# Kernel tuning notes

Hardware: AMD Instinct MI355X
Metric: run time of the kernel (lower is better)

Reference implementation:

```python
import jax, jax.numpy as jnp
import numpy as np

B = 512        # events (graphs) in batch
NPE = 512      # nodes per event (structured so knn can be batched)
N = B * NPE    # total nodes = 262144
K = 6          # knn neighbors
F_IN = 128     # 2 * n_samples
H = 16         # conv1 out
OUT = 10       # graph_out
COORD_MAX = 16 # detector grid extent


def setup_inputs() -> dict:
    key = jax.random.key(0)
    k1, k2, k3, k4 = jax.random.split(key, 4)
    xy = jax.random.randint(k1, (N, 2), 0, COORD_MAX, dtype=jnp.int32)
    batch = jnp.repeat(jnp.arange(B, dtype=jnp.int32), NPE)  # coo[:,2] = event id
    coo = jnp.concatenate([xy, batch[:, None]], axis=1)       # [N,3] int
    x = jax.random.normal(k2, (N, F_IN), dtype=jnp.float32)
    W1 = jax.random.normal(k3, (F_IN, H), dtype=jnp.float32) * (1.0 / np.sqrt(F_IN))
    b1 = jnp.zeros((H,), dtype=jnp.float32)
    W2 = jax.random.normal(k4, (H, OUT), dtype=jnp.float32) * (1.0 / np.sqrt(H))
    b2 = jnp.zeros((OUT,), dtype=jnp.float32)
    return {"coo": coo, "x": x, "W1": W1, "b1": b1, "W2": W2, "b2": b2}


def knn_edges(coo):
    # knn_graph(coo, K, batch=coo[:,2], loop=False): batches are contiguous
    # blocks of NPE nodes, so reshape and do per-event brute-force knn.
    pos = coo.astype(jnp.float32).reshape(B, NPE, 3)
    # squared pairwise distances per event: [B, n, n]
    d = jnp.sum((pos[:, :, None, :] - pos[:, None, :, :]) ** 2, axis=-1)
    d = d + jnp.eye(NPE, dtype=d.dtype) * 1e9  # exclude self (loop=False)
    _, idx = jax.lax.top_k(-d, K)              # [B, n, K] neighbor indices (local)
    base = (jnp.arange(B, dtype=jnp.int32) * NPE)[:, None, None]
    src = (idx.astype(jnp.int32) + base).reshape(-1)                       # j (neighbor)
    dst = jnp.broadcast_to(jnp.arange(NPE, dtype=jnp.int32)[None, :, None] + base,
                           (B, NPE, K)).reshape(-1)                        # i (center)
    return src, dst


def gcn_conv(x, W, b, src, dst):
    # GCNConv: out = D^{-1/2} (A + I) D^{-1/2} X W + b
    loops = jnp.arange(N, dtype=jnp.int32)
    row = jnp.concatenate([dst, loops])  # target
    col = jnp.concatenate([src, loops])  # source
    deg = jax.ops.segment_sum(jnp.ones_like(row, dtype=x.dtype), row, num_segments=N)
    dinv = jnp.where(deg > 0, jax.lax.rsqrt(deg), 0.0)
    norm = dinv[row] * dinv[col]         # [E]
    h = x @ W                            # [N, F_out]
    msg = h[col] * norm[:, None]         # gather + scale
    return jax.ops.segment_sum(msg, row, num_segments=N) + b


def reference(coo, x, W1, b1, W2, b2):
    src, dst = knn_edges(coo)
    h = jax.nn.relu(gcn_conv(x, W1, b1, src, dst))
    out = gcn_conv(h, W2, b2, src, dst)  # [N, OUT] per-node output (n_lin == 0)
    return out
```

## Files before the change

kernel.cpp:

```cpp
#include <hip/hip_runtime.h>
#include <hip/hip_bf16.h>

#define NPE   512
#define F_IN  128
#define HDIM  16
#define ODIM  10

typedef __attribute__((ext_vector_type(8))) short short8;
typedef __attribute__((ext_vector_type(4))) float f32x4;

static __device__ __forceinline__ unsigned pkbf(float lo, float hi) {
  __hip_bfloat162 h = __float22bfloat162_rn(make_float2(lo, hi));
  unsigned r;
  __builtin_memcpy(&r, &h, 4);
  return r;
}
static __device__ __forceinline__ short f2bf(float f) {
  __hip_bfloat16 h = __float2bfloat16(f);
  short r;
  __builtin_memcpy(&r, &h, 2);
  return r;
}
static __device__ __forceinline__ float bflo(unsigned d) {
  return __builtin_bit_cast(float, d << 16);
}
static __device__ __forceinline__ float bfhi(unsigned d) {
  return __builtin_bit_cast(float, d & 0xffff0000u);
}
static __device__ __forceinline__ unsigned umin2(unsigned a, unsigned b) { return a < b ? a : b; }
static __device__ __forceinline__ unsigned umax2(unsigned a, unsigned b) { return a > b ? a : b; }

__global__ __launch_bounds__(512, 4) void gnet_fused(
    const int* __restrict__ coo, const float* __restrict__ x,
    const float* __restrict__ W1, const float* __restrict__ b1,
    const float* __restrict__ W2, const float* __restrict__ b2,
    float* __restrict__ out)
{
  __shared__ __align__(16) short    hbuf[NPE][24];
  __shared__ __align__(16) short    stage_s[8][2048];
  __shared__ unsigned short cellof_s[NPE];
  __shared__ unsigned       cnt_s [256];
  __shared__ unsigned       scan_s[256];
  __shared__ unsigned       cur_s [256];
  __shared__ unsigned short bucket_s[NPE];
  __shared__ unsigned       top7_s[256][8];
  __shared__ unsigned       tile_c;
  __shared__ unsigned       sortflag;

  const int tid   = threadIdx.x;
  const int gbase = blockIdx.x * NPE;
  const int ln    = tid & 63;
  const int wv    = tid >> 6;
  const int lcol  = ln & 15;
  const int lkg   = ln >> 4;

  const int cx = coo[(gbase + tid) * 3 + 0];
  const int cy = coo[(gbase + tid) * 3 + 1];
  const int mycell = cy * 16 + cx;
  cellof_s[tid] = (unsigned short)mycell;
  if (tid == 0) { tile_c = 0; sortflag = 0; }
  __syncthreads();

  short8 bw1[4];
#pragma unroll
  for (int s = 0; s < 4; ++s) {
#pragma unroll
    for (int e = 0; e < 8; ++e) {
      const int k = s * 32 + lkg * 8 + e;
      bw1[s][e] = f2bf(W1[k * HDIM + lcol]);
    }
  }

  if (wv == 0) {
#pragma unroll
    for (int q = 0; q < 4; ++q) cnt_s[ln * 4 + q] = 0;
    __threadfence_block();
#pragma unroll
    for (int q = 0; q < 8; ++q)
      atomicAdd(&cnt_s[cellof_s[ln + q * 64]], 1u);
    __threadfence_block();
    const unsigned c0 = cnt_s[ln * 4 + 0], c1 = cnt_s[ln * 4 + 1];
    const unsigned c2 = cnt_s[ln * 4 + 2], c3 = cnt_s[ln * 4 + 3];
    const unsigned psum = c0 + c1 + c2 + c3;
    unsigned sv = psum;
#pragma unroll
    for (int off = 1; off < 64; off <<= 1) {
      unsigned u = __shfl_up(sv, off, 64);
      if (ln >= off) sv += u;
    }
    const unsigned basex = sv - psum;
    const unsigned e0 = basex + c0, e1 = e0 + c1, e2 = e1 + c2, e3 = e2 + c3;
    scan_s[ln * 4 + 0] = e0; cur_s[ln * 4 + 0] = e0 - c0;
    scan_s[ln * 4 + 1] = e1; cur_s[ln * 4 + 1] = e1 - c1;
    scan_s[ln * 4 + 2] = e2; cur_s[ln * 4 + 2] = e2 - c2;
    scan_s[ln * 4 + 3] = e3; cur_s[ln * 4 + 3] = e3 - c3;
    __threadfence_block();
#pragma unroll
    for (int q = 0; q < 8; ++q) {
      const int node = ln + q * 64;
      const unsigned slot = atomicAdd(&cur_s[cellof_s[node]], 1u);
      bucket_s[slot] = (unsigned short)node;
    }
    __threadfence_block();
    if (ln == 0) *(volatile unsigned*)&sortflag = 1u;
  } else if (wv < 4) {
    while (*(volatile unsigned*)&sortflag == 0u) __builtin_amdgcn_s_sleep(8);
    __threadfence_block();
  }

  if (wv < 4 && cnt_s[tid] != 0) {
    const int ccx = tid & 15, ccy = tid >> 4;
    unsigned k0 = 0x7fffffffu, k1 = k0, k2 = k0, k3 = k0, k4 = k0, k5 = k0, k6 = k0;
    auto insert7 = [&](unsigned key) {
      if (key < k6) {
        k6 = key;
        unsigned lo, hi;
        lo = umin2(k5, k6); hi = umax2(k5, k6); k5 = lo; k6 = hi;
        lo = umin2(k4, k5); hi = umax2(k4, k5); k4 = lo; k5 = hi;
        lo = umin2(k3, k4); hi = umax2(k3, k4); k3 = lo; k4 = hi;
        lo = umin2(k2, k3); hi = umax2(k2, k3); k2 = lo; k3 = hi;
        lo = umin2(k1, k2); hi = umax2(k1, k2); k1 = lo; k2 = hi;
        lo = umin2(k0, k1); hi = umax2(k0, k1); k0 = lo; k1 = hi;
      }
    };
    auto scan_cell = [&](int c, unsigned kb) {
      const unsigned e = scan_s[c];
      const unsigned n = cnt_s[c];
      for (unsigned q = e - n; q < e; ++q) insert7(kb | (unsigned)bucket_s[q]);
    };
    scan_cell(tid, 0u);
    for (int r = 1; r <= 15; ++r) {
      const unsigned r2 = (unsigned)(r * r);
      if (r2 > (k6 >> 9)) break;
      for (int sg = 0; sg < 2; ++sg) {
        const int yy = ccy + (sg ? r : -r);
        if (yy < 0 || yy > 15) continue;
        const int xlo = ccx - r < 0 ? 0 : ccx - r;
        const int xhi = ccx + r > 15 ? 15 : ccx + r;
        for (int xx = xlo; xx <= xhi; ++xx) {
          const int dx = xx - ccx;
          const unsigned kb = (unsigned)(dx * dx + (int)r2) << 9;
          if (kb < k6) scan_cell(yy * 16 + xx, kb);
        }
      }
      for (int sg = 0; sg < 2; ++sg) {
        const int xx = ccx + (sg ? r : -r);
        if (xx < 0 || xx > 15) continue;
        const int ylo = ccy - r + 1 < 0 ? 0 : ccy - r + 1;
        const int yhi = ccy + r - 1 > 15 ? 15 : ccy + r - 1;
        for (int yy = ylo; yy <= yhi; ++yy) {
          const int dy = yy - ccy;
          const unsigned kb = (unsigned)(dy * dy + (int)r2) << 9;
          if (kb < k6) scan_cell(yy * 16 + xx, kb);
        }
      }
    }
    unsigned* tp = top7_s[tid];
    tp[0] = k0; tp[1] = k1; tp[2] = k2; tp[3] = k3; tp[4] = k4; tp[5] = k5; tp[6] = k6;
  }

  {
    short* slab = &stage_s[wv][0];
    for (;;) {
      int t = 0;
      if (ln == 0) t = (int)atomicAdd(&tile_c, 1u);
      t = __shfl(t, 0, 64);
      if (t >= 32) break;
      const int rb = t * 16;
      const int srow = ln >> 5;
      const int scol = (ln & 31) * 4;
      float4 v[8];
#pragma unroll
      for (int j = 0; j < 8; ++j) {
        v[j] = *reinterpret_cast<const float4*>(
            x + (size_t)(gbase + rb + 2 * j + srow) * F_IN + scol);
      }
      __builtin_amdgcn_s_setprio(1);
#pragma unroll
      for (int j = 0; j < 8; ++j) {
        const unsigned lo = pkbf(v[j].x, v[j].y);
        const unsigned hi = pkbf(v[j].z, v[j].w);
        *reinterpret_cast<uint2*>(&slab[(2 * j + srow) * 128 + scol]) =
            make_uint2(lo, hi);
      }
      f32x4 acc = {0.f, 0.f, 0.f, 0.f};
#pragma unroll
      for (int s = 0; s < 4; ++s) {
        const short8 af = *reinterpret_cast<const short8*>(
            &slab[lcol * 128 + s * 32 + lkg * 8]);
        acc = __builtin_amdgcn_mfma_f32_16x16x32_bf16(af, bw1[s], acc, 0, 0, 0);
      }
#pragma unroll
      for (int i = 0; i < 4; ++i) {
        hbuf[rb + lkg * 4 + i][lcol] = f2bf(acc[i]);
      }
      __builtin_amdgcn_s_setprio(0);
    }
  }
  __syncthreads();

  short (*r_s)[16] = reinterpret_cast<short (*)[16]>(&stage_s[0][0]);

  const unsigned* tp = top7_s[mycell];
  const unsigned t0 = tp[0], t1 = tp[1], t2 = tp[2], t3 = tp[3];
  const unsigned t4 = tp[4], t5 = tp[5], t6 = tp[6];
  const unsigned selfkey = (unsigned)tid;
  int p = 7;
  p = (t6 == selfkey) ? 6 : p;
  p = (t5 == selfkey) ? 5 : p;
  p = (t4 == selfkey) ? 4 : p;
  p = (t3 == selfkey) ? 3 : p;
  p = (t2 == selfkey) ? 2 : p;
  p = (t1 == selfkey) ? 1 : p;
  p = (t0 == selfkey) ? 0 : p;
  const int nb0 = (int)((p > 0 ? t0 : t1) & 511u);
  const int nb1 = (int)((p > 1 ? t1 : t2) & 511u);
  const int nb2 = (int)((p > 2 ? t2 : t3) & 511u);
  const int nb3 = (int)((p > 3 ? t3 : t4) & 511u);
  const int nb4 = (int)((p > 4 ? t4 : t5) & 511u);
  const int nb5 = (int)((p > 5 ? t5 : t6) & 511u);
  const int rows[7] = {tid, nb0, nb1, nb2, nb3, nb4, nb5};

  {
    float acc[HDIM];
#pragma unroll
    for (int o = 0; o < HDIM; ++o) acc[o] = 0.f;
#pragma unroll
    for (int r = 0; r < 7; ++r) {
      const uint4* hp = reinterpret_cast<const uint4*>(&hbuf[rows[r]][0]);
      const uint4 ha = hp[0];
      const uint4 hb = hp[1];
      const unsigned hd[8] = {ha.x, ha.y, ha.z, ha.w, hb.x, hb.y, hb.z, hb.w};
#pragma unroll
      for (int q = 0; q < 8; ++q) {
        acc[2 * q]     += bflo(hd[q]);
        acc[2 * q + 1] += bfhi(hd[q]);
      }
    }
    const float inv = 1.0f / 7.0f;
    unsigned pk[8];
#pragma unroll
    for (int q = 0; q < 8; ++q) {
      const float v0 = fmaxf(acc[2 * q]     * inv + b1[2 * q],     0.f);
      const float v1 = fmaxf(acc[2 * q + 1] * inv + b1[2 * q + 1], 0.f);
      pk[q] = pkbf(v0, v1);
    }
    uint4* rp = reinterpret_cast<uint4*>(&r_s[tid][0]);
    rp[0] = make_uint4(pk[0], pk[1], pk[2], pk[3]);
    rp[1] = make_uint4(pk[4], pk[5], pk[6], pk[7]);
  }
  __syncthreads();

  {
    float acc[HDIM];
#pragma unroll
    for (int o = 0; o < HDIM; ++o) acc[o] = 0.f;
#pragma unroll
    for (int r = 0; r < 7; ++r) {
      const uint4* hp = reinterpret_cast<const uint4*>(&r_s[rows[r]][0]);
      const uint4 ha = hp[0];
      const uint4 hb = hp[1];
      const unsigned hd[8] = {ha.x, ha.y, ha.z, ha.w, hb.x, hb.y, hb.z, hb.w};
#pragma unroll
      for (int q = 0; q < 8; ++q) {
        acc[2 * q]     += bflo(hd[q]);
        acc[2 * q + 1] += bfhi(hd[q]);
      }
    }
    const float inv = 1.0f / 7.0f;
    unsigned pk[8];
#pragma unroll
    for (int q = 0; q < 8; ++q) {
      pk[q] = pkbf(acc[2 * q] * inv, acc[2 * q + 1] * inv);
    }
    uint4* ap = reinterpret_cast<uint4*>(&hbuf[tid][0]);
    ap[0] = make_uint4(pk[0], pk[1], pk[2], pk[3]);
    ap[1] = make_uint4(pk[4], pk[5], pk[6], pk[7]);
  }
  __syncthreads();

  {
    short8 bw2 = {0, 0, 0, 0, 0, 0, 0, 0};
    if (lkg < 2 && lcol < ODIM) {
#pragma unroll
      for (int e = 0; e < 8; ++e) {
        const int k = lkg * 8 + e;
        bw2[e] = f2bf(W2[k * ODIM + lcol]);
      }
    }
    const float b2v = (lcol < ODIM) ? b2[lcol] : 0.f;
#pragma unroll
    for (int t = 0; t < 4; ++t) {
      const int nt = wv * 64 + t * 16;
      short8 af = {0, 0, 0, 0, 0, 0, 0, 0};
      if (lkg < 2) {
        af = *reinterpret_cast<const short8*>(&hbuf[nt + lcol][lkg * 8]);
      }
      f32x4 acc = {0.f, 0.f, 0.f, 0.f};
      acc = __builtin_amdgcn_mfma_f32_16x16x32_bf16(af, bw2, acc, 0, 0, 0);
      if (lcol < ODIM) {
#pragma unroll
        for (int i = 0; i < 4; ++i) {
          __builtin_nontemporal_store(
              acc[i] + b2v,
              out + (size_t)(gbase + nt + lkg * 4 + i) * ODIM + lcol);
        }
      }
    }
  }
}

extern "C" void kernel_launch(void* const* d_in, const int* in_sizes, int n_in,
                              void* d_out, int out_size, void* d_ws, size_t ws_size,
                              hipStream_t stream) {
  const int*   coo = (const int*)  d_in[0];
  const float* x   = (const float*)d_in[1];
  const float* W1  = (const float*)d_in[2];
  const float* b1  = (const float*)d_in[3];
  const float* W2  = (const float*)d_in[4];
  const float* b2  = (const float*)d_in[5];
  gnet_fused<<<dim3(512), dim3(512), 0, stream>>>(coo, x, W1, b1, W2, b2,
                                                  (float*)d_out);
}
```

Measured before the change: 32.14 us.

## Widen block to twelve waves and split x tile loads into two halves

Raises the block from 8 to 12 wavefronts (768 threads) so more waves compete for the dynamic x-tile queue during the first GEMM stage. Only the first 512 threads do the per-node aggregation, and the output MFMA loop is redistributed across the 12 waves. The tile load is split into two batches of four float4 loads to cut register pressure, and hbuf padding is removed to save LDS. The cost is idle threads in the node phases and a larger LDS staging footprint, which may limit how many blocks fit per CU.

```diff
diff --git a/kernel.cpp b/kernel.cpp
--- a/kernel.cpp
+++ b/kernel.cpp
@@ -5,6 +5,8 @@
 #define F_IN  128
 #define HDIM  16
 #define ODIM  10
+#define NW    12
+#define NTHR  768
 
 typedef __attribute__((ext_vector_type(8))) short short8;
 typedef __attribute__((ext_vector_type(4))) float f32x4;
@@ -30,14 +32,14 @@
 static __device__ __forceinline__ unsigned umin2(unsigned a, unsigned b) { return a < b ? a : b; }
 static __device__ __forceinline__ unsigned umax2(unsigned a, unsigned b) { return a > b ? a : b; }
 
-__global__ __launch_bounds__(512, 4) void gnet_fused(
+__global__ __launch_bounds__(NTHR, 6) void gnet_fused(
     const int* __restrict__ coo, const float* __restrict__ x,
     const float* __restrict__ W1, const float* __restrict__ b1,
     const float* __restrict__ W2, const float* __restrict__ b2,
     float* __restrict__ out)
 {
-  __shared__ __align__(16) short    hbuf[NPE][24];
-  __shared__ __align__(16) short    stage_s[8][2048];
+  __shared__ __align__(16) short    hbuf[NPE][16];
+  __shared__ __align__(16) short    stage_s[NW][2048];
   __shared__ unsigned short cellof_s[NPE];
   __shared__ unsigned       cnt_s [256];
   __shared__ unsigned       scan_s[256];
@@ -53,11 +55,15 @@
   const int wv    = tid >> 6;
   const int lcol  = ln & 15;
   const int lkg   = ln >> 4;
-
-  const int cx = coo[(gbase + tid) * 3 + 0];
-  const int cy = coo[(gbase + tid) * 3 + 1];
-  const int mycell = cy * 16 + cx;
-  cellof_s[tid] = (unsigned short)mycell;
+  const bool node_th = (tid < NPE);
+
+  int mycell = 0;
+  if (node_th) {
+    const int cx0 = coo[(gbase + tid) * 3 + 0];
+    const int cy0 = coo[(gbase + tid) * 3 + 1];
+    mycell = cy0 * 16 + cx0;
+    cellof_s[tid] = (unsigned short)mycell;
+  }
   if (tid == 0) { tile_c = 0; sortflag = 0; }
   __syncthreads();
 
@@ -161,27 +167,32 @@
 
   {
     short* slab = &stage_s[wv][0];
+    const int srow = ln >> 5;
+    const int scol = (ln & 31) * 4;
     for (;;) {
       int t = 0;
       if (ln == 0) t = (int)atomicAdd(&tile_c, 1u);
       t = __shfl(t, 0, 64);
       if (t >= 32) break;
       const int rb = t * 16;
-      const int srow = ln >> 5;
-      const int scol = (ln & 31) * 4;
-      float4 v[8];
-#pragma unroll
-      for (int j = 0; j < 8; ++j) {
-        v[j] = *reinterpret_cast<const float4*>(
-            x + (size_t)(gbase + rb + 2 * j + srow) * F_IN + scol);
-      }
+      const float* xrow = x + (size_t)(gbase + rb + srow) * F_IN + scol;
+      float4 v[4];
+#pragma unroll
+      for (int j = 0; j < 4; ++j)
+        v[j] = *reinterpret_cast<const float4*>(xrow + (size_t)(2 * j) * F_IN);
       __builtin_amdgcn_s_setprio(1);
 #pragma unroll
-      for (int j = 0; j < 8; ++j) {
-        const unsigned lo = pkbf(v[j].x, v[j].y);
-        const unsigned hi = pkbf(v[j].z, v[j].w);
+      for (int j = 0; j < 4; ++j) {
         *reinterpret_cast<uint2*>(&slab[(2 * j + srow) * 128 + scol]) =
-            make_uint2(lo, hi);
+            make_uint2(pkbf(v[j].x, v[j].y), pkbf(v[j].z, v[j].w));
+      }
+#pragma unroll
+      for (int j = 0; j < 4; ++j)
+        v[j] = *reinterpret_cast<const float4*>(xrow + (size_t)(2 * j + 8) * F_IN);
+#pragma unroll
+      for (int j = 0; j < 4; ++j) {
+        *reinterpret_cast<uint2*>(&slab[(2 * j + 8 + srow) * 128 + scol]) =
+            make_uint2(pkbf(v[j].x, v[j].y), pkbf(v[j].z, v[j].w));
       }
       f32x4 acc = {0.f, 0.f, 0.f, 0.f};
 #pragma unroll
@@ -201,27 +212,30 @@
 
   short (*r_s)[16] = reinterpret_cast<short (*)[16]>(&stage_s[0][0]);
 
-  const unsigned* tp = top7_s[mycell];
-  const unsigned t0 = tp[0], t1 = tp[1], t2 = tp[2], t3 = tp[3];
-  const unsigned t4 = tp[4], t5 = tp[5], t6 = tp[6];
-  const unsigned selfkey = (unsigned)tid;
-  int p = 7;
-  p = (t6 == selfkey) ? 6 : p;
-  p = (t5 == selfkey) ? 5 : p;
-  p = (t4 == selfkey) ? 4 : p;
-  p = (t3 == selfkey) ? 3 : p;
-  p = (t2 == selfkey) ? 2 : p;
-  p = (t1 == selfkey) ? 1 : p;
-  p = (t0 == selfkey) ? 0 : p;
-  const int nb0 = (int)((p > 0 ? t0 : t1) & 511u);
-  const int nb1 = (int)((p > 1 ? t1 : t2) & 511u);
-  const int nb2 = (int)((p > 2 ? t2 : t3) & 511u);
-  const int nb3 = (int)((p > 3 ? t3 : t4) & 511u);
-  const int nb4 = (int)((p > 4 ? t4 : t5) & 511u);
-  const int nb5 = (int)((p > 5 ? t5 : t6) & 511u);
-  const int rows[7] = {tid, nb0, nb1, nb2, nb3, nb4, nb5};
-
-  {
+  int rows[7] = {0, 0, 0, 0, 0, 0, 0};
+  if (node_th) {
+    const unsigned* tp = top7_s[mycell];
+    const unsigned t0 = tp[0], t1 = tp[1], t2 = tp[2], t3 = tp[3];
+    const unsigned t4 = tp[4], t5 = tp[5], t6 = tp[6];
+    const unsigned selfkey = (unsigned)tid;
+    int p = 7;
+    p = (t6 == selfkey) ? 6 : p;
+    p = (t5 == selfkey) ? 5 : p;
+    p = (t4 == selfkey) ? 4 : p;
+    p = (t3 == selfkey) ? 3 : p;
+    p = (t2 == selfkey) ? 2 : p;
+    p = (t1 == selfkey) ? 1 : p;
+    p = (t0 == selfkey) ? 0 : p;
+    rows[0] = tid;
+    rows[1] = (int)((p > 0 ? t0 : t1) & 511u);
+    rows[2] = (int)((p > 1 ? t1 : t2) & 511u);
+    rows[3] = (int)((p > 2 ? t2 : t3) & 511u);
+    rows[4] = (int)((p > 3 ? t3 : t4) & 511u);
+    rows[5] = (int)((p > 4 ? t4 : t5) & 511u);
+    rows[6] = (int)((p > 5 ? t5 : t6) & 511u);
+  }
+
+  if (node_th) {
     float acc[HDIM];
 #pragma unroll
     for (int o = 0; o < HDIM; ++o) acc[o] = 0.f;
@@ -251,7 +265,7 @@
   }
   __syncthreads();
 
-  {
+  if (node_th) {
     float acc[HDIM];
 #pragma unroll
     for (int o = 0; o < HDIM; ++o) acc[o] = 0.f;
@@ -289,9 +303,8 @@
       }
     }
     const float b2v = (lcol < ODIM) ? b2[lcol] : 0.f;
-#pragma unroll
-    for (int t = 0; t < 4; ++t) {
-      const int nt = wv * 64 + t * 16;
+    for (int t = wv; t < 32; t += NW) {
+      const int nt = t * 16;
       short8 af = {0, 0, 0, 0, 0, 0, 0, 0};
       if (lkg < 2) {
         af = *reinterpret_cast<const short8*>(&hbuf[nt + lcol][lkg * 8]);
@@ -319,6 +332,6 @@
   const float* b1  = (const float*)d_in[3];
   const float* W2  = (const float*)d_in[4];
   const float* b2  = (const float*)d_in[5];
-  gnet_fused<<<dim3(512), dim3(512), 0, stream>>>(coo, x, W1, b1, W2, b2,
-                                                  (float*)d_out);
-}
+  gnet_fused<<<dim3(512), dim3(NTHR), 0, stream>>>(coo, x, W1, b1, W2, b2,
+                                                   (float*)d_out);
+}
```

New measurement: 35.71 us. 1.11x slower.

## Split fused kernel into knn/projection kernel and aggregation kernel via workspace

Applied to the files above, without the earlier changes.

Replaces the single fused per-event kernel with two launches. The first kernel runs heterogeneous blocks: 512 blocks each build one event's cell grid and kNN lists and write packed neighbor indices to global memory, while 2048 separate blocks stream x and compute the bf16 x@W1 projection with MFMA. The second kernel loads h1 and the neighbor lists and performs both aggregations and the W2 MFMA. This decouples the latency-bound kNN from the bandwidth-bound x stream so more blocks can keep memory busy, at the cost of an extra launch and a global round-trip for h1 and the neighbor indices.

```diff
diff --git a/kernel.cpp b/kernel.cpp
--- a/kernel.cpp
+++ b/kernel.cpp
@@ -5,6 +5,10 @@
 #define F_IN  128
 #define HDIM  16
 #define ODIM  10
+#define B_EV  512
+#define NTOT  (B_EV * NPE)
+#define KNNBLK 512
+#define STRBLK 2048
 
 typedef __attribute__((ext_vector_type(8))) short short8;
 typedef __attribute__((ext_vector_type(4))) float f32x4;
@@ -30,196 +34,215 @@
 static __device__ __forceinline__ unsigned umin2(unsigned a, unsigned b) { return a < b ? a : b; }
 static __device__ __forceinline__ unsigned umax2(unsigned a, unsigned b) { return a > b ? a : b; }
 
-__global__ __launch_bounds__(512, 4) void gnet_fused(
+__global__ __launch_bounds__(256, 6) void gnet_a(
     const int* __restrict__ coo, const float* __restrict__ x,
-    const float* __restrict__ W1, const float* __restrict__ b1,
-    const float* __restrict__ W2, const float* __restrict__ b2,
-    float* __restrict__ out)
+    const float* __restrict__ W1,
+    unsigned short* __restrict__ h1g,
+    uint4* __restrict__ nbg)
 {
-  __shared__ __align__(16) short    hbuf[NPE][24];
-  __shared__ __align__(16) short    stage_s[8][2048];
+  __shared__ __align__(16) short slab_s[4][2048];
   __shared__ unsigned short cellof_s[NPE];
-  __shared__ unsigned       cnt_s [256];
-  __shared__ unsigned       scan_s[256];
-  __shared__ unsigned       cur_s [256];
+  __shared__ unsigned cnt_s[256], scan_s[256], cur_s[256], wtot_s[4];
   __shared__ unsigned short bucket_s[NPE];
-  __shared__ unsigned       top7_s[256][8];
-  __shared__ unsigned       tile_c;
-  __shared__ unsigned       sortflag;
+
+  const int tid = threadIdx.x;
+  const int ln  = tid & 63;
+  const int wv  = tid >> 6;
+
+  if (blockIdx.x < KNNBLK) {
+    const int gbase = blockIdx.x * NPE;
+#pragma unroll
+    for (int q = 0; q < 2; ++q) {
+      const int node = tid + q * 256;
+      const int cx = coo[(gbase + node) * 3 + 0];
+      const int cy = coo[(gbase + node) * 3 + 1];
+      cellof_s[node] = (unsigned short)(cy * 16 + cx);
+    }
+    cnt_s[tid] = 0;
+    __syncthreads();
+    atomicAdd(&cnt_s[cellof_s[tid]], 1u);
+    atomicAdd(&cnt_s[cellof_s[tid + 256]], 1u);
+    __syncthreads();
+    unsigned sv = cnt_s[tid];
+#pragma unroll
+    for (int off = 1; off < 64; off <<= 1) {
+      unsigned u = __shfl_up(sv, off, 64);
+      if (ln >= off) sv += u;
+    }
+    if (ln == 63) wtot_s[wv] = sv;
+    __syncthreads();
+    unsigned add = 0;
+#pragma unroll
+    for (int w = 0; w < 3; ++w) if (w < wv) add += wtot_s[w];
+    sv += add;
+    scan_s[tid] = sv;
+    cur_s[tid]  = sv - cnt_s[tid];
+    __syncthreads();
+#pragma unroll
+    for (int q = 0; q < 2; ++q) {
+      const int node = tid + q * 256;
+      const unsigned slot = atomicAdd(&cur_s[cellof_s[node]], 1u);
+      bucket_s[slot] = (unsigned short)node;
+    }
+    __syncthreads();
+
+    const unsigned n = cnt_s[tid];
+    if (n) {
+      const int ccx = tid & 15, ccy = tid >> 4;
+      unsigned k0 = 0x7fffffffu, k1 = k0, k2 = k0, k3 = k0, k4 = k0, k5 = k0, k6 = k0;
+      auto insert7 = [&](unsigned key) {
+        if (key < k6) {
+          k6 = key;
+          unsigned lo, hi;
+          lo = umin2(k5, k6); hi = umax2(k5, k6); k5 = lo; k6 = hi;
+          lo = umin2(k4, k5); hi = umax2(k4, k5); k4 = lo; k5 = hi;
+          lo = umin2(k3, k4); hi = umax2(k3, k4); k3 = lo; k4 = hi;
+          lo = umin2(k2, k3); hi = umax2(k2, k3); k2 = lo; k3 = hi;
+          lo = umin2(k1, k2); hi = umax2(k1, k2); k1 = lo; k2 = hi;
+          lo = umin2(k0, k1); hi = umax2(k0, k1); k0 = lo; k1 = hi;
+        }
+      };
+      auto scan_cell = [&](int c, unsigned kb) {
+        const unsigned e = scan_s[c];
+        const unsigned m = cnt_s[c];
+        for (unsigned q = e - m; q < e; ++q) insert7(kb | (unsigned)bucket_s[q]);
+      };
+      scan_cell(tid, 0u);
+      for (int r = 1; r <= 15; ++r) {
+        const unsigned r2 = (unsigned)(r * r);
+        if (r2 > (k6 >> 9)) break;
+        for (int sg = 0; sg < 2; ++sg) {
+          const int yy = ccy + (sg ? r : -r);
+          if (yy < 0 || yy > 15) continue;
+          const int xlo = ccx - r < 0 ? 0 : ccx - r;
+          const int xhi = ccx + r > 15 ? 15 : ccx + r;
+          for (int xx = xlo; xx <= xhi; ++xx) {
+            const int dx = xx - ccx;
+            const unsigned kb = (unsigned)(dx * dx + (int)r2) << 9;
+            if (kb < k6) scan_cell(yy * 16 + xx, kb);
+          }
+        }
+        for (int sg = 0; sg < 2; ++sg) {
+          const int xx = ccx + (sg ? r : -r);
+          if (xx < 0 || xx > 15) continue;
+          const int ylo = ccy - r + 1 < 0 ? 0 : ccy - r + 1;
+          const int yhi = ccy + r - 1 > 15 ? 15 : ccy + r - 1;
+          for (int yy = ylo; yy <= yhi; ++yy) {
+            const int dy = yy - ccy;
+            const unsigned kb = (unsigned)(dy * dy + (int)r2) << 9;
+            if (kb < k6) scan_cell(yy * 16 + xx, kb);
+          }
+        }
+      }
+      const unsigned eend = scan_s[tid];
+      for (unsigned q = eend - n; q < eend; ++q) {
+        const unsigned node = bucket_s[q];
+        int p = 7;
+        p = (k6 == node) ? 6 : p;
+        p = (k5 == node) ? 5 : p;
+        p = (k4 == node) ? 4 : p;
+        p = (k3 == node) ? 3 : p;
+        p = (k2 == node) ? 2 : p;
+        p = (k1 == node) ? 1 : p;
+        p = (k0 == node) ? 0 : p;
+        const unsigned n0 = (p > 0 ? k0 : k1) & 511u;
+        const unsigned n1 = (p > 1 ? k1 : k2) & 511u;
+        const unsigned n2 = (p > 2 ? k2 : k3) & 511u;
+        const unsigned n3 = (p > 3 ? k3 : k4) & 511u;
+        const unsigned n4 = (p > 4 ? k4 : k5) & 511u;
+        const unsigned n5 = (p > 5 ? k5 : k6) & 511u;
+        uint4 pk;
+        pk.x = n0 | (n1 << 16);
+        pk.y = n2 | (n3 << 16);
+        pk.z = n4 | (n5 << 16);
+        pk.w = 0u;
+        nbg[gbase + node] = pk;
+      }
+    }
+  } else {
+    const int sb   = blockIdx.x - KNNBLK;
+    const int lcol = ln & 15;
+    const int lkg  = ln >> 4;
+    short8 bw1[4];
+#pragma unroll
+    for (int s = 0; s < 4; ++s) {
+#pragma unroll
+      for (int e = 0; e < 8; ++e) {
+        const int k = s * 32 + lkg * 8 + e;
+        bw1[s][e] = f2bf(W1[k * HDIM + lcol]);
+      }
+    }
+    short* slab = &slab_s[wv][0];
+    const int srow = ln >> 5;
+    const int scol = (ln & 31) * 4;
+    const int gw = sb * 128 + wv * 32;
+
+#pragma unroll
+    for (int half = 0; half < 2; ++half) {
+      const int gr = gw + half * 16;
+      const float* xrow = x + (size_t)(gr + srow) * F_IN + scol;
+      float4 v[4];
+#pragma unroll
+      for (int j = 0; j < 4; ++j)
+        v[j] = *reinterpret_cast<const float4*>(xrow + (size_t)(2 * j) * F_IN);
+#pragma unroll
+      for (int j = 0; j < 4; ++j)
+        *reinterpret_cast<uint2*>(&slab[(2 * j + srow) * 128 + scol]) =
+            make_uint2(pkbf(v[j].x, v[j].y), pkbf(v[j].z, v[j].w));
+#pragma unroll
+      for (int j = 0; j < 4; ++j)
+        v[j] = *reinterpret_cast<const float4*>(xrow + (size_t)(2 * j + 8) * F_IN);
+#pragma unroll
+      for (int j = 0; j < 4; ++j)
+        *reinterpret_cast<uint2*>(&slab[(2 * j + 8 + srow) * 128 + scol]) =
+            make_uint2(pkbf(v[j].x, v[j].y), pkbf(v[j].z, v[j].w));
+
+      f32x4 acc = {0.f, 0.f, 0.f, 0.f};
+#pragma unroll
+      for (int s = 0; s < 4; ++s) {
+        const short8 af = *reinterpret_cast<const short8*>(
+            &slab[lcol * 128 + s * 32 + lkg * 8]);
+        acc = __builtin_amdgcn_mfma_f32_16x16x32_bf16(af, bw1[s], acc, 0, 0, 0);
+      }
+#pragma unroll
+      for (int i = 0; i < 4; ++i)
+        slab[(lkg * 4 + i) * 16 + lcol] = f2bf(acc[i]);
+      asm volatile("s_waitcnt lgkmcnt(0)" ::: "memory");
+      const uint2 d = *reinterpret_cast<const uint2*>(&slab[ln * 4]);
+      *reinterpret_cast<uint2*>(h1g + (size_t)gr * 16 + ln * 4) = d;
+    }
+  }
+}
+
+__global__ __launch_bounds__(512, 4) void gnet_b(
+    const unsigned short* __restrict__ h1g, const uint4* __restrict__ nbg,
+    const float* __restrict__ b1, const float* __restrict__ W2,
+    const float* __restrict__ b2, float* __restrict__ out)
+{
+  __shared__ __align__(16) short h1_s[NPE][16];
+  __shared__ __align__(16) short r_s [NPE][16];
+  __shared__ __align__(16) short agg_s[NPE][16];
 
   const int tid   = threadIdx.x;
-  const int gbase = blockIdx.x * NPE;
   const int ln    = tid & 63;
   const int wv    = tid >> 6;
   const int lcol  = ln & 15;
   const int lkg   = ln >> 4;
-
-  const int cx = coo[(gbase + tid) * 3 + 0];
-  const int cy = coo[(gbase + tid) * 3 + 1];
-  const int mycell = cy * 16 + cx;
-  cellof_s[tid] = (unsigned short)mycell;
-  if (tid == 0) { tile_c = 0; sortflag = 0; }
+  const int gbase = blockIdx.x * NPE;
+
+  {
+    const uint4* src = reinterpret_cast<const uint4*>(h1g + (size_t)gbase * 16);
+    const uint4 a = src[tid * 2];
+    const uint4 b = src[tid * 2 + 1];
+    uint4* dst = reinterpret_cast<uint4*>(&h1_s[tid][0]);
+    dst[0] = a; dst[1] = b;
+  }
+  const uint4 nb = nbg[gbase + tid];
+  const int rows[7] = {tid,
+                       (int)(nb.x & 0xffffu), (int)(nb.x >> 16),
+                       (int)(nb.y & 0xffffu), (int)(nb.y >> 16),
+                       (int)(nb.z & 0xffffu), (int)(nb.z >> 16)};
   __syncthreads();
-
-  short8 bw1[4];
-#pragma unroll
-  for (int s = 0; s < 4; ++s) {
-#pragma unroll
-    for (int e = 0; e < 8; ++e) {
-      const int k = s * 32 + lkg * 8 + e;
-      bw1[s][e] = f2bf(W1[k * HDIM + lcol]);
-    }
-  }
-
-  if (wv == 0) {
-#pragma unroll
-    for (int q = 0; q < 4; ++q) cnt_s[ln * 4 + q] = 0;
-    __threadfence_block();
-#pragma unroll
-    for (int q = 0; q < 8; ++q)
-      atomicAdd(&cnt_s[cellof_s[ln + q * 64]], 1u);
-    __threadfence_block();
-    const unsigned c0 = cnt_s[ln * 4 + 0], c1 = cnt_s[ln * 4 + 1];
-    const unsigned c2 = cnt_s[ln * 4 + 2], c3 = cnt_s[ln * 4 + 3];
-    const unsigned psum = c0 + c1 + c2 + c3;
-    unsigned sv = psum;
-#pragma unroll
-    for (int off = 1; off < 64; off <<= 1) {
-      unsigned u = __shfl_up(sv, off, 64);
-      if (ln >= off) sv += u;
-    }
-    const unsigned basex = sv - psum;
-    const unsigned e0 = basex + c0, e1 = e0 + c1, e2 = e1 + c2, e3 = e2 + c3;
-    scan_s[ln * 4 + 0] = e0; cur_s[ln * 4 + 0] = e0 - c0;
-    scan_s[ln * 4 + 1] = e1; cur_s[ln * 4 + 1] = e1 - c1;
-    scan_s[ln * 4 + 2] = e2; cur_s[ln * 4 + 2] = e2 - c2;
-    scan_s[ln * 4 + 3] = e3; cur_s[ln * 4 + 3] = e3 - c3;
-    __threadfence_block();
-#pragma unroll
-    for (int q = 0; q < 8; ++q) {
-      const int node = ln + q * 64;
-      const unsigned slot = atomicAdd(&cur_s[cellof_s[node]], 1u);
-      bucket_s[slot] = (unsigned short)node;
-    }
-    __threadfence_block();
-    if (ln == 0) *(volatile unsigned*)&sortflag = 1u;
-  } else if (wv < 4) {
-    while (*(volatile unsigned*)&sortflag == 0u) __builtin_amdgcn_s_sleep(8);
-    __threadfence_block();
-  }
-
-  if (wv < 4 && cnt_s[tid] != 0) {
-    const int ccx = tid & 15, ccy = tid >> 4;
-    unsigned k0 = 0x7fffffffu, k1 = k0, k2 = k0, k3 = k0, k4 = k0, k5 = k0, k6 = k0;
-    auto insert7 = [&](unsigned key) {
-      if (key < k6) {
-        k6 = key;
-        unsigned lo, hi;
-        lo = umin2(k5, k6); hi = umax2(k5, k6); k5 = lo; k6 = hi;
-        lo = umin2(k4, k5); hi = umax2(k4, k5); k4 = lo; k5 = hi;
-        lo = umin2(k3, k4); hi = umax2(k3, k4); k3 = lo; k4 = hi;
-        lo = umin2(k2, k3); hi = umax2(k2, k3); k2 = lo; k3 = hi;
-        lo = umin2(k1, k2); hi = umax2(k1, k2); k1 = lo; k2 = hi;
-        lo = umin2(k0, k1); hi = umax2(k0, k1); k0 = lo; k1 = hi;
-      }
-    };
-    auto scan_cell = [&](int c, unsigned kb) {
-      const unsigned e = scan_s[c];
-      const unsigned n = cnt_s[c];
-      for (unsigned q = e - n; q < e; ++q) insert7(kb | (unsigned)bucket_s[q]);
-    };
-    scan_cell(tid, 0u);
-    for (int r = 1; r <= 15; ++r) {
-      const unsigned r2 = (unsigned)(r * r);
-      if (r2 > (k6 >> 9)) break;
-      for (int sg = 0; sg < 2; ++sg) {
-        const int yy = ccy + (sg ? r : -r);
-        if (yy < 0 || yy > 15) continue;
-        const int xlo = ccx - r < 0 ? 0 : ccx - r;
-        const int xhi = ccx + r > 15 ? 15 : ccx + r;
-        for (int xx = xlo; xx <= xhi; ++xx) {
-          const int dx = xx - ccx;
-          const unsigned kb = (unsigned)(dx * dx + (int)r2) << 9;
-          if (kb < k6) scan_cell(yy * 16 + xx, kb);
-        }
-      }
-      for (int sg = 0; sg < 2; ++sg) {
-        const int xx = ccx + (sg ? r : -r);
-        if (xx < 0 || xx > 15) continue;
-        const int ylo = ccy - r + 1 < 0 ? 0 : ccy - r + 1;
-        const int yhi = ccy + r - 1 > 15 ? 15 : ccy + r - 1;
-        for (int yy = ylo; yy <= yhi; ++yy) {
-          const int dy = yy - ccy;
-          const unsigned kb = (unsigned)(dy * dy + (int)r2) << 9;
-          if (kb < k6) scan_cell(yy * 16 + xx, kb);
-        }
-      }
-    }
-    unsigned* tp = top7_s[tid];
-    tp[0] = k0; tp[1] = k1; tp[2] = k2; tp[3] = k3; tp[4] = k4; tp[5] = k5; tp[6] = k6;
-  }
-
-  {
-    short* slab = &stage_s[wv][0];
-    for (;;) {
-      int t = 0;
-      if (ln == 0) t = (int)atomicAdd(&tile_c, 1u);
-      t = __shfl(t, 0, 64);
-      if (t >= 32) break;
-      const int rb = t * 16;
-      const int srow = ln >> 5;
-      const int scol = (ln & 31) * 4;
-      float4 v[8];
-#pragma unroll
-      for (int j = 0; j < 8; ++j) {
-        v[j] = *reinterpret_cast<const float4*>(
-            x + (size_t)(gbase + rb + 2 * j + srow) * F_IN + scol);
-      }
-      __builtin_amdgcn_s_setprio(1);
-#pragma unroll
-      for (int j = 0; j < 8; ++j) {
-        const unsigned lo = pkbf(v[j].x, v[j].y);
-        const unsigned hi = pkbf(v[j].z, v[j].w);
-        *reinterpret_cast<uint2*>(&slab[(2 * j + srow) * 128 + scol]) =
-            make_uint2(lo, hi);
-      }
-      f32x4 acc = {0.f, 0.f, 0.f, 0.f};
-#pragma unroll
-      for (int s = 0; s < 4; ++s) {
-        const short8 af = *reinterpret_cast<const short8*>(
-            &slab[lcol * 128 + s * 32 + lkg * 8]);
-        acc = __builtin_amdgcn_mfma_f32_16x16x32_bf16(af, bw1[s], acc, 0, 0, 0);
-      }
-#pragma unroll
-      for (int i = 0; i < 4; ++i) {
-        hbuf[rb + lkg * 4 + i][lcol] = f2bf(acc[i]);
-      }
-      __builtin_amdgcn_s_setprio(0);
-    }
-  }
-  __syncthreads();
-
-  short (*r_s)[16] = reinterpret_cast<short (*)[16]>(&stage_s[0][0]);
-
-  const unsigned* tp = top7_s[mycell];
-  const unsigned t0 = tp[0], t1 = tp[1], t2 = tp[2], t3 = tp[3];
-  const unsigned t4 = tp[4], t5 = tp[5], t6 = tp[6];
-  const unsigned selfkey = (unsigned)tid;
-  int p = 7;
-  p = (t6 == selfkey) ? 6 : p;
-  p = (t5 == selfkey) ? 5 : p;
-  p = (t4 == selfkey) ? 4 : p;
-  p = (t3 == selfkey) ? 3 : p;
-  p = (t2 == selfkey) ? 2 : p;
-  p = (t1 == selfkey) ? 1 : p;
-  p = (t0 == selfkey) ? 0 : p;
-  const int nb0 = (int)((p > 0 ? t0 : t1) & 511u);
-  const int nb1 = (int)((p > 1 ? t1 : t2) & 511u);
-  const int nb2 = (int)((p > 2 ? t2 : t3) & 511u);
-  const int nb3 = (int)((p > 3 ? t3 : t4) & 511u);
-  const int nb4 = (int)((p > 4 ? t4 : t5) & 511u);
-  const int nb5 = (int)((p > 5 ? t5 : t6) & 511u);
-  const int rows[7] = {tid, nb0, nb1, nb2, nb3, nb4, nb5};
 
   {
     float acc[HDIM];
@@ -227,7 +250,7 @@
     for (int o = 0; o < HDIM; ++o) acc[o] = 0.f;
 #pragma unroll
     for (int r = 0; r < 7; ++r) {
-      const uint4* hp = reinterpret_cast<const uint4*>(&hbuf[rows[r]][0]);
+      const uint4* hp = reinterpret_cast<const uint4*>(&h1_s[rows[r]][0]);
       const uint4 ha = hp[0];
       const uint4 hb = hp[1];
       const unsigned hd[8] = {ha.x, ha.y, ha.z, ha.w, hb.x, hb.y, hb.z, hb.w};
@@ -273,7 +296,7 @@
     for (int q = 0; q < 8; ++q) {
       pk[q] = pkbf(acc[2 * q] * inv, acc[2 * q + 1] * inv);
     }
-    uint4* ap = reinterpret_cast<uint4*>(&hbuf[tid][0]);
+    uint4* ap = reinterpret_cast<uint4*>(&agg_s[tid][0]);
     ap[0] = make_uint4(pk[0], pk[1], pk[2], pk[3]);
     ap[1] = make_uint4(pk[4], pk[5], pk[6], pk[7]);
   }
@@ -294,7 +317,7 @@
       const int nt = wv * 64 + t * 16;
       short8 af = {0, 0, 0, 0, 0, 0, 0, 0};
       if (lkg < 2) {
-        af = *reinterpret_cast<const short8*>(&hbuf[nt + lcol][lkg * 8]);
+        af = *reinterpret_cast<const short8*>(&agg_s[nt + lcol][lkg * 8]);
       }
       f32x4 acc = {0.f, 0.f, 0.f, 0.f};
       acc = __builtin_amdgcn_mfma_f32_16x16x32_bf16(af, bw2, acc, 0, 0, 0);
@@ -319,6 +342,10 @@
   const float* b1  = (const float*)d_in[3];
   const float* W2  = (const float*)d_in[4];
   const float* b2  = (const float*)d_in[5];
-  gnet_fused<<<dim3(512), dim3(512), 0, stream>>>(coo, x, W1, b1, W2, b2,
-                                                  (float*)d_out);
-}
+
+  unsigned short* h1g = (unsigned short*)d_ws;
+  uint4*          nbg = (uint4*)((char*)d_ws + (size_t)NTOT * 16 * 2);
+
+  gnet_a<<<dim3(KNNBLK + STRBLK), dim3(256), 0, stream>>>(coo, x, W1, h1g, nbg);
+  gnet_b<<<dim3(B_EV), dim3(512), 0, stream>>>(h1g, nbg, b1, W2, b2, (float*)d_out);
+}
```

Result: slower. 36.49 us (+13.5%).
